# Kernel tuning notes

Hardware: AMD Instinct MI355X
Metric: run time of the kernel (lower is better)

The kernel has to match this reference:

```python
import jax, jax.numpy as jnp
import numpy as np

B, S, D = 8, 2048, 1024          # batch, seq, d_model
E, H = 32, 128                   # n_experts_ffn, d_expert_ffn
SHARED, K = 2, 4                 # n_expert_shared_ffn, k_ffn (routed top-k)
R = E - SHARED                   # n_expert_routed_ffn


def setup_inputs() -> dict:
    key = jax.random.key(0)
    ks = jax.random.split(key, 5)
    token_stream = jax.random.normal(ks[0], (B, S, D), jnp.float32)
    selection_input = jax.random.normal(ks[1], (B, S, D), jnp.float32)
    # init scaling mirrors reset_parameters (std_scale = 1)
    keys = jax.random.normal(ks[2], (E, D, H), jnp.float32) / np.sqrt(D)
    values = jax.random.normal(ks[3], (E, H, D), jnp.float32) / np.sqrt(E * H)
    expert_sel = jax.random.normal(ks[4], (E, D), jnp.float32) / np.sqrt(D)
    bias_ffn = jnp.zeros((E,), jnp.float32)
    return {
        "token_stream": token_stream,
        "selection_input": selection_input,
        "keys": keys,
        "values": values,
        "expert_sel": expert_sel,
        "bias_ffn": bias_ffn,
    }


def reference(token_stream, selection_input, keys, values, expert_sel, bias_ffn):
    # Router: sigmoid affinity over all experts. [B,S,E]
    affinity = jax.nn.sigmoid(jnp.einsum("bsd,ed->bse", selection_input, expert_sel))

    # Top-k over routed experts only (bias-corrected scores pick INDICES only).
    routed_scores = affinity[..., :R] + bias_ffn[:R]
    _, sel_routed = jax.lax.top_k(routed_scores, K)            # [B,S,K] int32
    shared = jnp.broadcast_to(jnp.arange(R, E, dtype=sel_routed.dtype),
                              sel_routed.shape[:-1] + (SHARED,))
    sel = jnp.concatenate([sel_routed, shared], axis=-1)        # [B,S,K+SHARED]

    # Gather the (unbiased) affinities of the selected experts.
    aff_sel = jnp.take_along_axis(affinity, sel, axis=-1)       # [B,S,K+SHARED]

    # Per-token dense combine weight over experts: w[b,s,e] = affinity if e selected else 0.
    # (selected indices are distinct: topk indices in [0,R), shared in [R,E))
    w = jnp.sum(jax.nn.one_hot(sel, E, dtype=affinity.dtype) * aff_sel[..., None],
                axis=-2)                                        # [B,S,E]

    # Expert FFN: cvmm(x, sel, keys) -> silu -> cvmm(., sel, values) weighted by affinity.
    # Dense-masked equivalent: compute all experts, zero out unselected via w.
    h = jax.nn.silu(jnp.einsum("bsd,edh->bseh", token_stream, keys))  # [B,S,E,H]
    out = jnp.einsum("bseh,bse,ehd->bsd", h, w, values)               # [B,S,D]
    return out, sel
```

## Files before the change

### kernel.cpp

```cpp
#include <hip/hip_runtime.h>
#include <math.h>

#define NTOK   16384
#define DDIM   1024
#define HDIM   128
#define NEXP   32
#define NROUTE 30
#define TOPK   4
#define TS     64
#define NJOBS_F 1696
#define CPX_F   212
#define SLAB   ((size_t)NTOK * DDIM)
#define NB_ROUTER 512
#define NB_FUSED  (NB_ROUTER + 4608)

typedef short bf16x8 __attribute__((ext_vector_type(8)));
typedef float f32x16 __attribute__((ext_vector_type(16)));
typedef unsigned int u32x4 __attribute__((ext_vector_type(4)));
typedef unsigned short u16;

__device__ __forceinline__ float sigmoidf_(float x) { return 1.f / (1.f + expf(-x)); }

__device__ __forceinline__ u16 f2bf(float x) {
  unsigned u = __float_as_uint(x);
  u += 0x7fffu + ((u >> 16) & 1u);
  return (u16)(u >> 16);
}
__device__ __forceinline__ float bf2f(u16 v) {
  return __uint_as_float(((unsigned)v) << 16);
}

__device__ __forceinline__ f32x16 mfma32(uint4 a, uint4 b, f32x16 c) {
  union { uint4 u; bf16x8 h; } A, B;
  A.u = a; B.u = b;
  return __builtin_amdgcn_mfma_f32_32x32x16_bf16(A.h, B.h, c, 0, 0, 0);
}

__device__ __forceinline__ void gload16(const void* g, void* l) {
  __builtin_amdgcn_global_load_lds(
      (const __attribute__((address_space(1))) unsigned int*)g,
      (__attribute__((address_space(3))) unsigned int*)l, 16, 0, 0);
}

__device__ __forceinline__ void lgkm_bar() {
  asm volatile("s_waitcnt lgkmcnt(0)\ns_barrier" ::: "memory");
}

__global__ __launch_bounds__(256, 2) void prep_router_kernel(
    const float* __restrict__ X, u16* __restrict__ Xb,
    const float* __restrict__ K, u16* __restrict__ Kf,
    const float* __restrict__ V, u16* __restrict__ Vf,
    const float* __restrict__ SI, const float* __restrict__ ES,
    const float* __restrict__ bias, float* __restrict__ out_sel,
    float* __restrict__ w6, int* __restrict__ sel_e, int* __restrict__ counts)
{
  __shared__ __align__(16) char lds[66048];
  const int tid = threadIdx.x;

  if (blockIdx.x < NB_ROUTER) {
    const int wave = tid >> 6, lane = tid & 63;
    const int tok0 = blockIdx.x * 32 + wave * 8;
    float (*pbuf)[65] = ((float (*)[65])lds) + wave * 32;
    float (*aff)[33]  = (float (*)[33])(lds + 33280);
    int* hist = (int*)(lds + 37504);

    if (tid < 128) hist[tid] = 0;

    float x[8][16];
#pragma unroll
    for (int t = 0; t < 8; ++t) {
      const float* xp = SI + (size_t)(tok0 + t) * DDIM + lane * 4;
#pragma unroll
      for (int s = 0; s < 4; ++s) {
        const float4 v = *(const float4*)(xp + s * 256);
        x[t][s*4+0]=v.x; x[t][s*4+1]=v.y; x[t][s*4+2]=v.z; x[t][s*4+3]=v.w;
      }
    }

#pragma unroll
    for (int g = 0; g < 8; ++g) {
#pragma unroll
      for (int ei = 0; ei < 4; ++ei) {
        const int e = g * 4 + ei;
        float es[16];
        const float* ep = ES + (size_t)e * DDIM + lane * 4;
#pragma unroll
        for (int s = 0; s < 4; ++s) {
          const float4 v = *(const float4*)(ep + s * 256);
          es[s*4+0]=v.x; es[s*4+1]=v.y; es[s*4+2]=v.z; es[s*4+3]=v.w;
        }
#pragma unroll
        for (int t = 0; t < 8; ++t) {
          float p = 0.f;
#pragma unroll
          for (int u = 0; u < 16; ++u) p = fmaf(x[t][u], es[u], p);
          pbuf[ei * 8 + t][lane] = p;
        }
      }
      const int pr = lane & 31, hf = lane >> 5;
      const float* src = &pbuf[pr][hf * 32];
      float4 s4 = make_float4(0.f, 0.f, 0.f, 0.f);
#pragma unroll
      for (int j = 0; j < 8; ++j) {
        const float4 v = *(const float4*)(src + j * 4);
        s4.x += v.x; s4.y += v.y; s4.z += v.z; s4.w += v.w;
      }
      float s = (s4.x + s4.y) + (s4.z + s4.w);
      s += __shfl_xor(s, 32, 64);
      if (hf == 0) aff[wave * 8 + (pr & 7)][g * 4 + (pr >> 3)] = s;
    }
    __syncthreads();

    if (lane < 8) {
      const int tok = tok0 + lane;
      float af[NEXP];
#pragma unroll
      for (int e2 = 0; e2 < NEXP; ++e2)
        af[e2] = sigmoidf_(aff[wave * 8 + lane][e2]);
      float sc[NROUTE];
#pragma unroll
      for (int e2 = 0; e2 < NROUTE; ++e2) sc[e2] = af[e2] + bias[e2];
      unsigned used = 0u;
      int idx[6];
#pragma unroll
      for (int j = 0; j < TOPK; ++j) {
        float bv = -1e30f; int best = 0;
#pragma unroll
        for (int e2 = 0; e2 < NROUTE; ++e2)
          if (!((used >> e2) & 1u) && sc[e2] > bv) { bv = sc[e2]; best = e2; }
        used |= (1u << best);
        idx[j] = best;
      }
      idx[4] = 30; idx[5] = 31;
#pragma unroll
      for (int j = 0; j < 6; ++j) {
        out_sel[(size_t)tok * 6 + j] = (float)idx[j];
        w6[(size_t)tok * 6 + j] = af[idx[j]];
      }
#pragma unroll
      for (int j = 0; j < TOPK; ++j) {
        sel_e[(size_t)tok * TOPK + j] = idx[j];
        atomicAdd(&hist[j * NEXP + idx[j]], 1);
      }
    }
    __syncthreads();
    if (tid < 128) {
      const int c = hist[tid];
      if (c) atomicAdd(&counts[tid], c);
    }
    return;
  }

  int b = blockIdx.x - NB_ROUTER;
  float (*t)[129] = (float (*)[129])lds;

  if (b < 4096) {
    const size_t base = ((size_t)b * 256 + tid) * 16;
    u16 v[16];
#pragma unroll
    for (int i = 0; i < 4; ++i) {
      const float4 f = *(const float4*)(X + base + i * 4);
      v[i*4+0] = f2bf(f.x); v[i*4+1] = f2bf(f.y);
      v[i*4+2] = f2bf(f.z); v[i*4+3] = f2bf(f.w);
    }
    *(uint4*)(Xb + base) = *(const uint4*)v;
    *(uint4*)(Xb + base + 8) = *(const uint4*)(v + 8);
    return;
  }
  b -= 4096;
  if (b < 256) {
    const int kc = b & 7, e = b >> 3;
#pragma unroll
    for (int i = 0; i < 64; ++i) {
      const int g = tid + i * 256;
      const int d = g >> 7, h = g & 127;
      t[d][h] = K[((size_t)e * DDIM + kc * 128 + d) * HDIM + h];
    }
    __syncthreads();
    u16* dst = Kf + ((size_t)e * 8 + kc) * 16384;
#pragma unroll
    for (int i = 0; i < 64; ++i) {
      const int f = tid + i * 256;
      const int s = f >> 11, wn = (f >> 9) & 3, l = (f >> 3) & 63, j = f & 7;
      const int khalf = l >> 5, l31 = l & 31;
      dst[f] = f2bf(t[(s * 2 + khalf) * 8 + j][wn * 32 + l31]);
    }
    return;
  }
  b -= 256;
  {
    const int dc = b & 7, e = b >> 3;
#pragma unroll
    for (int i = 0; i < 64; ++i) {
      const int g = tid + i * 256;
      const int h = g >> 7, dl = g & 127;
      t[h][dl] = V[((size_t)e * HDIM + h) * DDIM + dc * 128 + dl];
    }
    __syncthreads();
    u16* dst = Vf + ((size_t)e * 8 + dc) * 16384;
#pragma unroll
    for (int i = 0; i < 64; ++i) {
      const int f = tid + i * 256;
      const int s = f >> 11, wn = (f >> 9) & 3, l = (f >> 3) & 63, j = f & 7;
      const int khalf = l >> 5, l31 = l & 31;
      dst[f] = f2bf(t[(s * 2 + khalf) * 8 + j][wn * 32 + l31]);
    }
  }
}

__global__ __launch_bounds__(256) void scan_kernel(const int* __restrict__ counts,
                                                   int* __restrict__ offsets,
                                                   int4* __restrict__ jm)
{
  __shared__ int c4[30][4];
  __shared__ int off4[30][4];
  __shared__ int nch[32];
  __shared__ int joff[31];
  const int tid = threadIdx.x;

  if (tid < 4) {
    int off = 0;
    for (int e = 0; e < NROUTE; ++e) {
      const int c = counts[tid * NEXP + e];
      offsets[tid * NEXP + e] = off;
      c4[e][tid] = c; off4[e][tid] = off;
      off += c;
    }
  }
  __syncthreads();
  if (tid < NROUTE) {
    int n = 0;
#pragma unroll
    for (int r = 0; r < 4; ++r) n += (c4[tid][r] + TS - 1) / TS;
    nch[tid] = n;
  }
  __syncthreads();
  if (tid == 0) {
    int run = 0;
    for (int e = 0; e < NROUTE; ++e) { joff[e] = run; run += nch[e]; }
    joff[NROUTE] = run;
  }
  __syncthreads();
  const int rt = joff[NROUTE];

  if (tid < NROUTE) {
    const int e = tid;
    int idx = joff[e];
    for (int r = 0; r < 4; ++r) {
      const int c = c4[e][r];
      for (int ch = 0; ch * TS < c; ++ch)
        jm[idx++] = make_int4(e, off4[e][r] + ch * TS, min(TS, c - ch * TS), r);
    }
  }
  for (int i = tid; i < 512; i += 256)
    jm[rt + i] = make_int4(30 + (i >> 8), (i & 255) * TS, TS, 4 + (i >> 8));
  for (int i = rt + 512 + tid; i < NJOBS_F; i += 256)
    jm[i] = make_int4(0, 0, 0, 0);
}

__global__ __launch_bounds__(256) void scatter_kernel(
    const int* __restrict__ sel_e, const float* __restrict__ w6,
    const int* __restrict__ offsets, int* __restrict__ cursor,
    int* __restrict__ list_tok, float* __restrict__ list_w)
{
  const int t = blockIdx.x * 256 + threadIdx.x;
  if (t >= NTOK) return;
#pragma unroll
  for (int j = 0; j < TOPK; ++j) {
    const int e   = sel_e[(size_t)t * TOPK + j];
    const int pos = atomicAdd(&cursor[j * NEXP + e], 1);
    const int dst = j * NTOK + offsets[j * NEXP + e] + pos;
    list_tok[dst] = t;
    list_w[dst]   = w6[(size_t)t * 6 + j];
  }
  list_tok[4 * NTOK + t] = t; list_w[4 * NTOK + t] = w6[(size_t)t * 6 + 4];
  list_tok[5 * NTOK + t] = t; list_w[5 * NTOK + t] = w6[(size_t)t * 6 + 5];
}

__device__ __forceinline__ void loadb(uint4* b, const u16* __restrict__ base,
                                      int c, int wid, int lane) {
#pragma unroll
  for (int s = 0; s < 8; ++s)
    b[s] = *(const uint4*)(base + (size_t)(((c * 8 + s) * 4 + wid) * 512) + lane * 8);
}

__global__ __launch_bounds__(256, 2) void ffn_kernel(
    const u16* __restrict__ Xb, const u16* __restrict__ Kf, const u16* __restrict__ Vf,
    const int4* __restrict__ jm, const int* __restrict__ list_tok,
    const float* __restrict__ list_w, u16* __restrict__ part)
{
  __shared__ __align__(16) u16 Xs[2][8192];
  __shared__ __align__(16) u16 Hs[TS * 128];
  __shared__ int   s_tok[TS];
  __shared__ float s_w[TS];

  const int bid = blockIdx.x;
  const int4 J = jm[(bid & 7) * CPX_F + (bid >> 3)];
  const int nrow = J.z;
  if (nrow == 0) return;
  const int e = J.x, base = J.y, rank = J.w;
  const int tid = threadIdx.x;
  const int wid = tid >> 6, lane = tid & 63;
  const int l31 = lane & 31, khalf = lane >> 5;
  const int sx = l31 & 15;

  const u16* Kf_e = Kf + (size_t)e * 131072;
  const u16* Vf_e = Vf + (size_t)e * 131072;
  const int*   lt  = list_tok + rank * NTOK + base;
  const float* lww = list_w  + rank * NTOK + base;

  size_t srcoff[4];
#pragma unroll
  for (int u = 0; u < 4; ++u) {
    const int r  = wid * 16 + u * 4 + (lane >> 4);
    const int rr = (r < nrow) ? r : 0;
    srcoff[u] = (size_t)lt[rr] * DDIM + (size_t)(((lane & 15) ^ (r & 15)) << 3);
  }

  #define STAGE_A(kc_, buf_) do { \
    _Pragma("unroll") \
    for (int u_ = 0; u_ < 4; ++u_) \
      gload16(Xb + srcoff[u_] + (kc_) * 128, &Xs[buf_][(wid * 16 + u_ * 4) * 128]); \
  } while (0)

  uint4 bb[2][8];
  STAGE_A(0, 0);
  loadb(bb[0], Kf_e, 0, wid, lane);

  if (tid < TS) {
    int t = 0; float w = 0.f;
    if (tid < nrow) { t = lt[tid]; w = lww[tid]; }
    s_tok[tid] = t; s_w[tid] = w;
  }
  lgkm_bar();

  f32x16 acc0, acc1;
#pragma unroll
  for (int i = 0; i < 16; ++i) { acc0[i] = 0.f; acc1[i] = 0.f; }

#pragma unroll
  for (int kc = 0; kc < 8; ++kc) {
    const int cur = kc & 1;
    asm volatile("s_barrier" ::: "memory");
    __builtin_amdgcn_sched_barrier(0);
    if (kc < 7) { STAGE_A(kc + 1, cur ^ 1); loadb(bb[cur ^ 1], Kf_e, kc + 1, wid, lane); }
    else        { loadb(bb[cur ^ 1], Vf_e, 0, wid, lane); }
    if (kc < 7) asm volatile("s_waitcnt vmcnt(12)" ::: "memory");
    else        asm volatile("s_waitcnt vmcnt(8)"  ::: "memory");
    asm volatile("s_barrier" ::: "memory");
    __builtin_amdgcn_sched_barrier(0);
#pragma unroll
    for (int s = 0; s < 8; ++s) {
      const int so = (((s * 2 + khalf) ^ sx) << 3);
      const uint4 a0 = *(const uint4*)(&Xs[cur][l31 * 128 + so]);
      const uint4 a1 = *(const uint4*)(&Xs[cur][(32 + l31) * 128 + so]);
      acc0 = mfma32(a0, bb[cur][s], acc0);
      acc1 = mfma32(a1, bb[cur][s], acc1);
    }
  }

  {
    const int hcol = wid * 32 + l31;
#pragma unroll
    for (int r = 0; r < 16; ++r) {
      const int row0 = (r & 3) + 8 * (r >> 2) + 4 * khalf;
      float v0 = acc0[r];
      v0 = v0 / (1.f + expf(-v0)) * s_w[row0];
      Hs[row0 * 128 + ((((hcol >> 3) ^ (row0 & 15)) << 3) | (hcol & 7))] = f2bf(v0);
      const int row1 = row0 + 32;
      float v1 = acc1[r];
      v1 = v1 / (1.f + expf(-v1)) * s_w[row1];
      Hs[row1 * 128 + ((((hcol >> 3) ^ (row1 & 15)) << 3) | (hcol & 7))] = f2bf(v1);
    }
  }
  lgkm_bar();

  uint4 a20[8], a21[8];
#pragma unroll
  for (int s = 0; s < 8; ++s) {
    a20[s] = *(const uint4*)(Hs + l31 * 128 + (((s * 2 + khalf) ^ sx) << 3));
    a21[s] = *(const uint4*)(Hs + (32 + l31) * 128 + (((s * 2 + khalf) ^ sx) << 3));
  }

  unsigned ob0[16], ob1[16]; bool ov0[16], ov1[16];
#pragma unroll
  for (int r = 0; r < 16; ++r) {
    const int row0 = (r & 3) + 8 * (r >> 2) + 4 * khalf;
    const int row1 = row0 + 32;
    ov0[r] = row0 < nrow; ov1[r] = row1 < nrow;
    ob0[r] = (unsigned)s_tok[row0] * DDIM;
    ob1[r] = (unsigned)s_tok[row1] * DDIM;
  }

  u16* pp = part + (size_t)rank * SLAB;

#pragma unroll
  for (int dc = 0; dc < 8; ++dc) {
    const int cur = dc & 1;
    if (dc < 7) loadb(bb[cur ^ 1], Vf_e, dc + 1, wid, lane);
    f32x16 o0, o1;
#pragma unroll
    for (int i = 0; i < 16; ++i) { o0[i] = 0.f; o1[i] = 0.f; }
#pragma unroll
    for (int s = 0; s < 8; ++s) {
      o0 = mfma32(a20[s], bb[cur][s], o0);
      o1 = mfma32(a21[s], bb[cur][s], o1);
    }
    const int col = dc * 128 + wid * 32 + l31;
#pragma unroll
    for (int r = 0; r < 16; ++r) {
      if (ov0[r]) __builtin_nontemporal_store(f2bf(o0[r]), &pp[(size_t)ob0[r] + col]);
      if (ov1[r]) __builtin_nontemporal_store(f2bf(o1[r]), &pp[(size_t)ob1[r] + col]);
    }
  }
  #undef STAGE_A
}

__global__ __launch_bounds__(256) void reduce_kernel(const u16* __restrict__ part,
                                                     float* __restrict__ out)
{
  const size_t i8 = ((size_t)blockIdx.x * 256 + threadIdx.x) * 8;
  float s[8];
#pragma unroll
  for (int j = 0; j < 8; ++j) s[j] = 0.f;
#pragma unroll
  for (int r = 0; r < 6; ++r) {
    const u32x4 v = __builtin_nontemporal_load((const u32x4*)(part + r * SLAB + i8));
#pragma unroll
    for (int q = 0; q < 4; ++q) {
      s[q*2+0] += __uint_as_float((v[q] & 0xffffu) << 16);
      s[q*2+1] += __uint_as_float(v[q] & 0xffff0000u);
    }
  }
  float4 o0 = make_float4(s[0], s[1], s[2], s[3]);
  float4 o1 = make_float4(s[4], s[5], s[6], s[7]);
  *(float4*)(out + i8) = o0;
  *(float4*)(out + i8 + 4) = o1;
}

extern "C" void kernel_launch(void* const* d_in, const int* in_sizes, int n_in,
                              void* d_out, int out_size, void* d_ws, size_t ws_size,
                              hipStream_t stream)
{
  const float* X    = (const float*)d_in[0];
  const float* SI   = (const float*)d_in[1];
  const float* keys = (const float*)d_in[2];
  const float* vals = (const float*)d_in[3];
  const float* ES   = (const float*)d_in[4];
  const float* bias = (const float*)d_in[5];
  float* out = (float*)d_out;
  float* out_sel = out + SLAB;

  char* ws = (char*)d_ws;
  int*   counts   = (int*)(ws + 0);
  int*   cursor   = (int*)(ws + 512);
  int*   offsets  = (int*)(ws + 1024);
  int4*  jm       = (int4*)(ws + 2048);
  int*   list_tok = (int*)(ws + 57344);
  float* list_w   = (float*)(ws + 450560);
  float* w6       = (float*)(ws + 919552);
  int*   sel_e    = (int*)(ws + 1312768);
  u16*   Xb       = (u16*)(ws + 1576960);
  u16*   Kf       = (u16*)(ws + 35131392);
  u16*   Vf       = (u16*)(ws + 43520000);
  u16*   part     = (u16*)(ws + 51908608);

  hipMemsetAsync(counts, 0, 1024, stream);

  prep_router_kernel<<<NB_FUSED, 256, 0, stream>>>(X, Xb, keys, Kf, vals, Vf,
                                                   SI, ES, bias, out_sel, w6,
                                                   sel_e, counts);
  scan_kernel<<<1, 256, 0, stream>>>(counts, offsets, jm);
  scatter_kernel<<<NTOK / 256, 256, 0, stream>>>(sel_e, w6, offsets, cursor, list_tok, list_w);
  ffn_kernel<<<NJOBS_F, 256, 0, stream>>>(Xb, Kf, Vf, jm, list_tok, list_w, part);
  reduce_kernel<<<SLAB / (256 * 8), 256, 0, stream>>>(part, out);
}
```

Measured before the change: 336.6 us.

## Fuse both shared experts into one FFN job sharing the token tile

Shared experts 30 and 31 were separate jobs, each writing its own bf16 partial slab. Now one job per 64-token tile computes both experts in sequence and reuses the token indices and weights. It preloads expert 31's first key tile and X chunk during expert 30's down-projection, then accumulates expert 31's output into the same slab with a read-modify-write. This removes one partial slab, so the reduce reads 5 slabs instead of 6, and drops the scatter writes for the shared ranks. The cost is an extra bf16 rounding step and longer shared-expert blocks, which may unbalance the schedule.

New measurement: 912.5 us. 171% more time.

```diff
diff --git a/kernel.cpp b/kernel.cpp
--- a/kernel.cpp
+++ b/kernel.cpp
@@ -252,9 +252,8 @@
         jm[idx++] = make_int4(e, off4[e][r] + ch * TS, min(TS, c - ch * TS), r);
     }
   }
-  for (int i = tid; i < 512; i += 256)
-    jm[rt + i] = make_int4(30 + (i >> 8), (i & 255) * TS, TS, 4 + (i >> 8));
-  for (int i = rt + 512 + tid; i < NJOBS_F; i += 256)
+  jm[rt + tid] = make_int4(30, tid * TS, TS, 4);
+  for (int i = rt + 256 + tid; i < NJOBS_F; i += 256)
     jm[i] = make_int4(0, 0, 0, 0);
 }
 
@@ -273,8 +272,6 @@
     list_tok[dst] = t;
     list_w[dst]   = w6[(size_t)t * 6 + j];
   }
-  list_tok[4 * NTOK + t] = t; list_w[4 * NTOK + t] = w6[(size_t)t * 6 + 4];
-  list_tok[5 * NTOK + t] = t; list_w[5 * NTOK + t] = w6[(size_t)t * 6 + 5];
 }
 
 __device__ __forceinline__ void loadb(uint4* b, const u16* __restrict__ base,
@@ -287,25 +284,25 @@
 __global__ __launch_bounds__(256, 2) void ffn_kernel(
     const u16* __restrict__ Xb, const u16* __restrict__ Kf, const u16* __restrict__ Vf,
     const int4* __restrict__ jm, const int* __restrict__ list_tok,
-    const float* __restrict__ list_w, u16* __restrict__ part)
+    const float* __restrict__ list_w, const float* __restrict__ w6,
+    u16* __restrict__ part)
 {
   __shared__ __align__(16) u16 Xs[2][8192];
   __shared__ __align__(16) u16 Hs[TS * 128];
   __shared__ int   s_tok[TS];
-  __shared__ float s_w[TS];
+  __shared__ float s_w[TS], s_w2[TS];
 
   const int bid = blockIdx.x;
   const int4 J = jm[(bid & 7) * CPX_F + (bid >> 3)];
   const int nrow = J.z;
   if (nrow == 0) return;
-  const int e = J.x, base = J.y, rank = J.w;
+  const int e0 = J.x, base = J.y, rank = J.w;
+  const bool sh2 = (rank == 4);
   const int tid = threadIdx.x;
   const int wid = tid >> 6, lane = tid & 63;
   const int l31 = lane & 31, khalf = lane >> 5;
   const int sx = l31 & 15;
 
-  const u16* Kf_e = Kf + (size_t)e * 131072;
-  const u16* Vf_e = Vf + (size_t)e * 131072;
   const int*   lt  = list_tok + rank * NTOK + base;
   const float* lww = list_w  + rank * NTOK + base;
 
@@ -314,7 +311,8 @@
   for (int u = 0; u < 4; ++u) {
     const int r  = wid * 16 + u * 4 + (lane >> 4);
     const int rr = (r < nrow) ? r : 0;
-    srcoff[u] = (size_t)lt[rr] * DDIM + (size_t)(((lane & 15) ^ (r & 15)) << 3);
+    const int tk = sh2 ? (base + rr) : lt[rr];
+    srcoff[u] = (size_t)tk * DDIM + (size_t)(((lane & 15) ^ (r & 15)) << 3);
   }
 
   #define STAGE_A(kc_, buf_) do { \
@@ -325,62 +323,15 @@
 
   uint4 bb[2][8];
   STAGE_A(0, 0);
-  loadb(bb[0], Kf_e, 0, wid, lane);
+  loadb(bb[0], Kf + (size_t)e0 * 131072, 0, wid, lane);
 
   if (tid < TS) {
-    int t = 0; float w = 0.f;
-    if (tid < nrow) { t = lt[tid]; w = lww[tid]; }
-    s_tok[tid] = t; s_w[tid] = w;
+    int t = 0; float w = 0.f, w2 = 0.f;
+    if (sh2) { t = base + tid; w = w6[(size_t)t * 6 + 4]; w2 = w6[(size_t)t * 6 + 5]; }
+    else if (tid < nrow) { t = lt[tid]; w = lww[tid]; }
+    s_tok[tid] = t; s_w[tid] = w; s_w2[tid] = w2;
   }
   lgkm_bar();
-
-  f32x16 acc0, acc1;
-#pragma unroll
-  for (int i = 0; i < 16; ++i) { acc0[i] = 0.f; acc1[i] = 0.f; }
-
-#pragma unroll
-  for (int kc = 0; kc < 8; ++kc) {
-    const int cur = kc & 1;
-    asm volatile("s_barrier" ::: "memory");
-    __builtin_amdgcn_sched_barrier(0);
-    if (kc < 7) { STAGE_A(kc + 1, cur ^ 1); loadb(bb[cur ^ 1], Kf_e, kc + 1, wid, lane); }
-    else        { loadb(bb[cur ^ 1], Vf_e, 0, wid, lane); }
-    if (kc < 7) asm volatile("s_waitcnt vmcnt(12)" ::: "memory");
-    else        asm volatile("s_waitcnt vmcnt(8)"  ::: "memory");
-    asm volatile("s_barrier" ::: "memory");
-    __builtin_amdgcn_sched_barrier(0);
-#pragma unroll
-    for (int s = 0; s < 8; ++s) {
-      const int so = (((s * 2 + khalf) ^ sx) << 3);
-      const uint4 a0 = *(const uint4*)(&Xs[cur][l31 * 128 + so]);
-      const uint4 a1 = *(const uint4*)(&Xs[cur][(32 + l31) * 128 + so]);
-      acc0 = mfma32(a0, bb[cur][s], acc0);
-      acc1 = mfma32(a1, bb[cur][s], acc1);
-    }
-  }
-
-  {
-    const int hcol = wid * 32 + l31;
-#pragma unroll
-    for (int r = 0; r < 16; ++r) {
-      const int row0 = (r & 3) + 8 * (r >> 2) + 4 * khalf;
-      float v0 = acc0[r];
-      v0 = v0 / (1.f + expf(-v0)) * s_w[row0];
-      Hs[row0 * 128 + ((((hcol >> 3) ^ (row0 & 15)) << 3) | (hcol & 7))] = f2bf(v0);
-      const int row1 = row0 + 32;
-      float v1 = acc1[r];
-      v1 = v1 / (1.f + expf(-v1)) * s_w[row1];
-      Hs[row1 * 128 + ((((hcol >> 3) ^ (row1 & 15)) << 3) | (hcol & 7))] = f2bf(v1);
-    }
-  }
-  lgkm_bar();
-
-  uint4 a20[8], a21[8];
-#pragma unroll
-  for (int s = 0; s < 8; ++s) {
-    a20[s] = *(const uint4*)(Hs + l31 * 128 + (((s * 2 + khalf) ^ sx) << 3));
-    a21[s] = *(const uint4*)(Hs + (32 + l31) * 128 + (((s * 2 + khalf) ^ sx) << 3));
-  }
 
   unsigned ob0[16], ob1[16]; bool ov0[16], ov1[16];
 #pragma unroll
@@ -392,25 +343,94 @@
     ob1[r] = (unsigned)s_tok[row1] * DDIM;
   }
 
-  u16* pp = part + (size_t)rank * SLAB;
-
-#pragma unroll
-  for (int dc = 0; dc < 8; ++dc) {
-    const int cur = dc & 1;
-    if (dc < 7) loadb(bb[cur ^ 1], Vf_e, dc + 1, wid, lane);
-    f32x16 o0, o1;
-#pragma unroll
-    for (int i = 0; i < 16; ++i) { o0[i] = 0.f; o1[i] = 0.f; }
+  u16* pp = part + (size_t)(sh2 ? 4 : rank) * SLAB;
+  const int nee = sh2 ? 2 : 1;
+
+  for (int ee = 0; ee < nee; ++ee) {
+    const u16* Kf_e = Kf + (size_t)(e0 + ee) * 131072;
+    const u16* Vf_e = Vf + (size_t)(e0 + ee) * 131072;
+
+    f32x16 acc0, acc1;
+#pragma unroll
+    for (int i = 0; i < 16; ++i) { acc0[i] = 0.f; acc1[i] = 0.f; }
+
+#pragma unroll
+    for (int kc = 0; kc < 8; ++kc) {
+      const int cur = kc & 1;
+      asm volatile("s_barrier" ::: "memory");
+      __builtin_amdgcn_sched_barrier(0);
+      if (kc < 7) { STAGE_A(kc + 1, cur ^ 1); loadb(bb[cur ^ 1], Kf_e, kc + 1, wid, lane); }
+      else        { loadb(bb[cur ^ 1], Vf_e, 0, wid, lane); }
+      if (kc < 7) asm volatile("s_waitcnt vmcnt(12)" ::: "memory");
+      else        asm volatile("s_waitcnt vmcnt(8)"  ::: "memory");
+      asm volatile("s_barrier" ::: "memory");
+      __builtin_amdgcn_sched_barrier(0);
+#pragma unroll
+      for (int s = 0; s < 8; ++s) {
+        const int so = (((s * 2 + khalf) ^ sx) << 3);
+        const uint4 a0 = *(const uint4*)(&Xs[cur][l31 * 128 + so]);
+        const uint4 a1 = *(const uint4*)(&Xs[cur][(32 + l31) * 128 + so]);
+        acc0 = mfma32(a0, bb[cur][s], acc0);
+        acc1 = mfma32(a1, bb[cur][s], acc1);
+      }
+    }
+
+    {
+      const int hcol = wid * 32 + l31;
+      const float* swp = ee ? s_w2 : s_w;
+#pragma unroll
+      for (int r = 0; r < 16; ++r) {
+        const int row0 = (r & 3) + 8 * (r >> 2) + 4 * khalf;
+        float v0 = acc0[r];
+        v0 = v0 / (1.f + expf(-v0)) * swp[row0];
+        Hs[row0 * 128 + ((((hcol >> 3) ^ (row0 & 15)) << 3) | (hcol & 7))] = f2bf(v0);
+        const int row1 = row0 + 32;
+        float v1 = acc1[r];
+        v1 = v1 / (1.f + expf(-v1)) * swp[row1];
+        Hs[row1 * 128 + ((((hcol >> 3) ^ (row1 & 15)) << 3) | (hcol & 7))] = f2bf(v1);
+      }
+    }
+    lgkm_bar();
+
+    uint4 a20[8], a21[8];
 #pragma unroll
     for (int s = 0; s < 8; ++s) {
-      o0 = mfma32(a20[s], bb[cur][s], o0);
-      o1 = mfma32(a21[s], bb[cur][s], o1);
-    }
-    const int col = dc * 128 + wid * 32 + l31;
-#pragma unroll
-    for (int r = 0; r < 16; ++r) {
-      if (ov0[r]) __builtin_nontemporal_store(f2bf(o0[r]), &pp[(size_t)ob0[r] + col]);
-      if (ov1[r]) __builtin_nontemporal_store(f2bf(o1[r]), &pp[(size_t)ob1[r] + col]);
+      a20[s] = *(const uint4*)(Hs + l31 * 128 + (((s * 2 + khalf) ^ sx) << 3));
+      a21[s] = *(const uint4*)(Hs + (32 + l31) * 128 + (((s * 2 + khalf) ^ sx) << 3));
+    }
+
+#pragma unroll
+    for (int dc = 0; dc < 8; ++dc) {
+      const int cur = dc & 1;
+      if (dc < 7) loadb(bb[cur ^ 1], Vf_e, dc + 1, wid, lane);
+      else if (sh2 && ee == 0) loadb(bb[cur ^ 1], Kf + (size_t)31 * 131072, 0, wid, lane);
+      if (dc == 6 && sh2 && ee == 0) STAGE_A(0, 0);
+      f32x16 o0, o1;
+#pragma unroll
+      for (int i = 0; i < 16; ++i) { o0[i] = 0.f; o1[i] = 0.f; }
+#pragma unroll
+      for (int s = 0; s < 8; ++s) {
+        o0 = mfma32(a20[s], bb[cur][s], o0);
+        o1 = mfma32(a21[s], bb[cur][s], o1);
+      }
+      const int col = dc * 128 + wid * 32 + l31;
+#pragma unroll
+      for (int r = 0; r < 16; ++r) {
+        if (ov0[r]) {
+          const size_t p = (size_t)ob0[r] + col;
+          if (sh2) {
+            if (ee == 0) pp[p] = f2bf(o0[r]);
+            else __builtin_nontemporal_store(f2bf(bf2f(pp[p]) + o0[r]), &pp[p]);
+          } else __builtin_nontemporal_store(f2bf(o0[r]), &pp[p]);
+        }
+        if (ov1[r]) {
+          const size_t p = (size_t)ob1[r] + col;
+          if (sh2) {
+            if (ee == 0) pp[p] = f2bf(o1[r]);
+            else __builtin_nontemporal_store(f2bf(bf2f(pp[p]) + o1[r]), &pp[p]);
+          } else __builtin_nontemporal_store(f2bf(o1[r]), &pp[p]);
+        }
+      }
     }
   }
   #undef STAGE_A
@@ -424,7 +444,7 @@
 #pragma unroll
   for (int j = 0; j < 8; ++j) s[j] = 0.f;
 #pragma unroll
-  for (int r = 0; r < 6; ++r) {
+  for (int r = 0; r < 5; ++r) {
     const u32x4 v = __builtin_nontemporal_load((const u32x4*)(part + r * SLAB + i8));
 #pragma unroll
     for (int q = 0; q < 4; ++q) {
@@ -472,6 +492,6 @@
                                                    sel_e, counts);
   scan_kernel<<<1, 256, 0, stream>>>(counts, offsets, jm);
   scatter_kernel<<<NTOK / 256, 256, 0, stream>>>(sel_e, w6, offsets, cursor, list_tok, list_w);
-  ffn_kernel<<<NJOBS_F, 256, 0, stream>>>(Xb, Kf, Vf, jm, list_tok, list_w, part);
+  ffn_kernel<<<NJOBS_F, 256, 0, stream>>>(Xb, Kf, Vf, jm, list_tok, list_w, w6, part);
   reduce_kernel<<<SLAB / (256 * 8), 256, 0, stream>>>(part, out);
 }
```
